# Kernel tuning notes

Measured on AMD Instinct MI355X. Metric: run time of the kernel, lower is better.

The kernel has to match this reference:

```python
import jax, jax.numpy as jnp
import numpy as np
import math

B, S, H, NH = 2, 2048, 1024, 16
HD = H // NH


def setup_inputs() -> dict:
    key = jax.random.key(0)
    k1, k2, k3 = jax.random.split(key, 3)
    hidden_states = jax.random.normal(k1, (B, S, H), dtype=jnp.float32)
    attention_mask = jnp.zeros((B, 1, 1, S), dtype=jnp.float32)
    w_qkv = jax.random.normal(k2, (3 * H, H), dtype=jnp.float32) * (1.0 / math.sqrt(H))
    w_out = jax.random.normal(k3, (H, H), dtype=jnp.float32) * (1.0 / math.sqrt(H))
    gate = jnp.ones((NH,), dtype=jnp.float32)
    return {"hidden_states": hidden_states, "attention_mask": attention_mask,
            "w_qkv": w_qkv, "w_out": w_out, "gate": gate}


def reference(hidden_states, attention_mask, w_qkv, w_out, gate):
    b, s, h = hidden_states.shape
    nh, hd = NH, HD
    # fused QKV projection (no bias)
    qkv = hidden_states @ w_qkv.T                      # [b, s, 3h]
    qkv = qkv.reshape(b, s, 3, nh, hd)
    q, k, v = jnp.moveaxis(qkv, 2, 0)                  # each [b, s, nh, hd]
    q = q.transpose(0, 2, 1, 3)                        # [b, nh, s, hd]
    k = k.transpose(0, 2, 1, 3)
    v = v.transpose(0, 2, 1, 3)
    scores = jnp.einsum('bhqd,bhkd->bhqk', q, k) / math.sqrt(hd)
    scores = scores + attention_mask                   # broadcast [b,1,1,s]
    probs = jax.nn.softmax(scores, axis=-1)            # dropout p=0 -> identity
    ctx = jnp.einsum('bhqk,bhkd->bhqd', probs, v)      # [b, nh, s, hd]
    ctx = ctx.transpose(0, 2, 1, 3)                    # [b, s, nh, hd]
    ctx = ctx * gate[None, None, :, None]              # per-head gating
    ctx = ctx.reshape(b, s, h)
    out = ctx @ w_out.T
    # all gates active (> 1e-4) -> active_gates/num_heads == 1, no rescale
    return out
```

## Files before the change

### kernel.cpp

```cpp
#include <hip/hip_runtime.h>
#include <stdint.h>


typedef __attribute__((ext_vector_type(8))) short short8;
typedef __attribute__((ext_vector_type(4))) float floatx4;
typedef __attribute__((ext_vector_type(4))) unsigned int uint4v;
typedef __attribute__((ext_vector_type(2))) unsigned int uint2v;

__device__ __forceinline__ unsigned short f2bf(float f) {
    unsigned int u = __float_as_uint(f);
    unsigned int r = u + 0x7fffu + ((u >> 16) & 1u);
    return (unsigned short)(r >> 16);
}
#if __has_builtin(__builtin_amdgcn_cvt_pk_bf16_f32)
__device__ __forceinline__ unsigned int pack_bf2(float lo, float hi) {
    auto v = __builtin_amdgcn_cvt_pk_bf16_f32(lo, hi);
    return __builtin_bit_cast(unsigned int, v);
}
#else
__device__ __forceinline__ unsigned int pack_bf2(float lo, float hi) {
    unsigned int a = __float_as_uint(lo) + 0x8000u;
    unsigned int b = __float_as_uint(hi) + 0x8000u;
    return __builtin_amdgcn_perm(b, a, 0x07060302u);
}
#endif

#if __has_builtin(__builtin_amdgcn_exp2f)
#define EXP2(x) __builtin_amdgcn_exp2f(x)
#else
#define EXP2(x) exp2f(x)
#endif

__device__ __forceinline__ void gl2lds16(const void* g, void* l) {
    __builtin_amdgcn_global_load_lds(
        (const __attribute__((address_space(1))) unsigned int*)g,
        (__attribute__((address_space(3))) unsigned int*)l, 16, 0, 0);
}

#define MFMA32(a, b, c) __builtin_amdgcn_mfma_f32_16x16x32_bf16((a), (b), (c), 0, 0, 0)

__global__ __launch_bounds__(256)
void cvt_all(const float* __restrict__ a, const float* __restrict__ b,
             const float* __restrict__ c, const float* __restrict__ mask,
             unsigned short* __restrict__ oa, unsigned short* __restrict__ ob,
             unsigned short* __restrict__ oc, float* __restrict__ m2b)
{
    int i = blockIdx.x * 256 + threadIdx.x;
    if (i >= 2097152) {
        int off = i - 2097152;
        float4 v = *(const float4*)(mask + (size_t)off * 4);
        const float L2E = 1.44269504f, C2 = -14.4269504f;
        float4 w;
        w.x = fmaf(v.x, L2E, C2); w.y = fmaf(v.y, L2E, C2);
        w.z = fmaf(v.z, L2E, C2); w.w = fmaf(v.w, L2E, C2);
        *(float4*)(m2b + (size_t)off * 4) = w;
        return;
    }
    const float* src; unsigned short* dst; int off;
    if (i < 1048576)      { src = a; dst = oa; off = i; }
    else if (i < 1835008) { src = b; dst = ob; off = i - 1048576; }
    else                  { src = c; dst = oc; off = i - 1835008; }
    float4 v = *(const float4*)(src + (size_t)off * 4);
    uint2v w;
    w[0] = pack_bf2(v.x, v.y);
    w[1] = pack_bf2(v.z, v.w);
    *(uint2v*)(dst + (size_t)off * 4) = w;
}

template<int MODE, int BN>
__global__ __launch_bounds__(256)
void gemm_nt(const unsigned short* __restrict__ A,
             const unsigned short* __restrict__ Bm,
             unsigned short* __restrict__ out0,
             unsigned short* __restrict__ out1,
             unsigned short* __restrict__ out2,
             float* __restrict__ outf,
             int N)
{
    constexpr int BUFB  = 8192 + BN * 64;
    constexpr int NSTEP = 32;
    constexpr int NA    = 2;
    constexpr int NB    = BN / 64;
    constexpr int BSL   = BN / 32;
    __shared__ unsigned char smem[3 * BUFB];
    const int K = 1024;
    const int tid  = threadIdx.x;
    const int wave = tid >> 6, lane = tid & 63;
    const int l15  = lane & 15, quad = lane >> 4;
    const int wm = wave >> 1, wn = wave & 1;

    int Lid = blockIdx.y * gridDim.x + blockIdx.x;
    int bm = (Lid & 7) * 4 + ((Lid >> 3) & 3);
    int bn = Lid >> 5;

    floatx4 acc[4][BSL];
#pragma unroll
    for (int i = 0; i < 4; i++)
#pragma unroll
        for (int j = 0; j < BSL; j++)
            acc[i][j] = floatx4{0.f, 0.f, 0.f, 0.f};

    int soffA[NA], soffB[NB];
#pragma unroll
    for (int l = 0; l < NA; l++) {
        int s = (wave * NA + l) * 64 + lane;
        int L = s >> 3, q = (s & 7) ^ (L & 7);
        soffA[l] = (L * 2 + (q >> 2)) * K + (q & 3) * 8;
    }
#pragma unroll
    for (int l = 0; l < NB; l++) {
        int s = (wave * NB + l) * 64 + lane;
        int L = s >> 3, q = (s & 7) ^ (L & 7);
        soffB[l] = (L * 2 + (q >> 2)) * K + (q & 3) * 8;
    }
    int aoff[4], boff[BSL];
#pragma unroll
    for (int i = 0; i < 4; i++) {
        int r = wm * 64 + i * 16 + l15, L = r >> 1;
        aoff[i] = L * 128 + (((((r & 1) << 2) | quad) ^ (L & 7)) * 16);
    }
#pragma unroll
    for (int j = 0; j < BSL; j++) {
        int r = wn * (BN / 2) + j * 16 + l15, L = r >> 1;
        boff[j] = 8192 + L * 128 + (((((r & 1) << 2) | quad) ^ (L & 7)) * 16);
    }

    const unsigned short* Abase = A  + (size_t)(bm * 128) * K;
    const unsigned short* Bbase = Bm + (size_t)(bn * BN) * K;

    auto STAGE = [&](int u, int bufb) {
        const int k0 = u * 32;
#pragma unroll
        for (int l = 0; l < NA; l++)
            gl2lds16(Abase + (size_t)soffA[l] + k0, &smem[bufb + (wave * NA + l) * 1024]);
#pragma unroll
        for (int l = 0; l < NB; l++)
            gl2lds16(Bbase + (size_t)soffB[l] + k0, &smem[bufb + 8192 + (wave * NB + l) * 1024]);
    };

    STAGE(0, 0);
    STAGE(1, BUFB);

    int b0 = 0, b2 = 2;
    for (int t = 0; t < NSTEP; t++) {
        asm volatile("" ::: "memory");
        __builtin_amdgcn_s_barrier();
        asm volatile("" ::: "memory");
        if (t + 2 < NSTEP) {
            STAGE(t + 2, b2 * BUFB);
            if (BN == 128) asm volatile("s_waitcnt vmcnt(8)" ::: "memory");
            else           asm volatile("s_waitcnt vmcnt(6)" ::: "memory");
        } else if (t + 2 == NSTEP) {
            if (BN == 128) asm volatile("s_waitcnt vmcnt(4)" ::: "memory");
            else           asm volatile("s_waitcnt vmcnt(3)" ::: "memory");
        } else {
            asm volatile("s_waitcnt vmcnt(0)" ::: "memory");
        }
        __builtin_amdgcn_s_barrier();
        asm volatile("" ::: "memory");

        const int cb = b0 * BUFB;
        short8 af[4], bfr[BSL];
#pragma unroll
        for (int i = 0; i < 4; i++)
            af[i] = *(const short8*)(&smem[cb + aoff[i]]);
#pragma unroll
        for (int j = 0; j < BSL; j++)
            bfr[j] = *(const short8*)(&smem[cb + boff[j]]);
#pragma unroll
        for (int i = 0; i < 4; i++)
#pragma unroll
            for (int j = 0; j < BSL; j++)
                acc[i][j] = MFMA32(af[i], bfr[j], acc[i][j]);

        b0 = (b0 == 2) ? 0 : b0 + 1;
        b2 = (b2 == 2) ? 0 : b2 + 1;
    }

#pragma unroll
    for (int i = 0; i < 4; i++) {
#pragma unroll
        for (int j = 0; j < BSL; j++) {
            int n = bn * BN + wn * (BN / 2) + j * 16 + l15;
#pragma unroll
            for (int r = 0; r < 4; r++) {
                int m = bm * 128 + wm * 64 + i * 16 + quad * 4 + r;
                float fv = acc[i][j][r];
                if (MODE == 1) {
                    outf[(size_t)m * N + n] = fv;
                } else {
                    int t = n >> 10;
                    int h = (n >> 6) & 15;
                    int d = n & 63;
                    int b = m >> 11, si = m & 2047;
                    if (t == 2) {
                        int sip = (si & ~31) | (((si >> 2) & 3) << 3)
                                | (((si >> 4) & 1) << 2) | (si & 3);
                        out2[(((size_t)(b * 16 + h)) * 64 + d) * 2048 + sip] = f2bf(fv);
                    } else {
                        if (t == 0) fv *= 0.18033688f;
                        size_t off = (((size_t)(b * 16 + h)) * 2048 + si) * 64 + d;
                        unsigned short* dst = (t == 0) ? out0 : out1;
                        dst[off] = f2bf(fv);
                    }
                }
            }
        }
    }
}

__global__ __launch_bounds__(256, 2)
void attn_kernel(const unsigned short* __restrict__ Qb,
                 const unsigned short* __restrict__ Kb,
                 const unsigned short* __restrict__ VbT,
                 const float* __restrict__ m2b,
                 const float* __restrict__ gateb,
                 unsigned short* __restrict__ ctx)
{
    __shared__ unsigned char smem[16384];
    const int S = 2048;
    const int tid  = threadIdx.x;
    const int wave = tid >> 6, lane = tid & 63;
    const int l15  = lane & 15, quad = lane >> 4;

    int Lid = blockIdx.y * gridDim.x + blockIdx.x;
    int bh = (Lid & 7) * 4 + ((Lid >> 3) & 3);
    int qc = Lid >> 5;
    const int b = bh >> 4, h = bh & 15;
    const int q0 = qc * 128 + wave * 32;

    const size_t headoff = (size_t)bh * S * 64;
    const unsigned short* Qh  = Qb  + headoff;
    const unsigned short* Kh  = Kb  + headoff;
    const unsigned short* VhT = VbT + headoff;
    const float* m2p = m2b + (size_t)b * S;

    int koff, voff;
    {
        int s = wave * 64 + lane;
        int key = s >> 3;
        koff = key * 64 + (((s & 7) ^ (key & 7)) * 8);
        int L = s >> 3, q = (s & 7) ^ (L & 7);
        voff = (L * 2 + (q >> 2)) * 2048 + (q & 3) * 8;
    }
    int qkoff[2];
#pragma unroll
    for (int s2 = 0; s2 < 2; s2++)
        qkoff[s2] = l15 * 128 + (((s2 * 4 + quad) ^ (l15 & 7)) * 16);
    const int pvoff = 4096 + (l15 >> 1) * 128
                    + (((((l15 & 1) << 2) | quad) ^ ((l15 >> 1) & 7)) * 16);

    short8 aq[2][2];
#pragma unroll
    for (int sub = 0; sub < 2; sub++)
#pragma unroll
        for (int s2 = 0; s2 < 2; s2++)
            aq[sub][s2] = *(const short8*)(Qh + (size_t)(q0 + sub * 16 + l15) * 64 + s2 * 32 + quad * 8);

    floatx4 o[2][4];
    floatx4 lq[2];
#pragma unroll
    for (int sub = 0; sub < 2; sub++) {
        lq[sub] = floatx4{0.f, 0.f, 0.f, 0.f};
#pragma unroll
        for (int dt = 0; dt < 4; dt++) o[sub][dt] = floatx4{0.f, 0.f, 0.f, 0.f};
    }

    const uint4v onesu = {0x3F803F80u, 0x3F803F80u, 0x3F803F80u, 0x3F803F80u};
    const short8 ONES = __builtin_bit_cast(short8, onesu);

    gl2lds16(Kh + koff, &smem[wave * 1024]);
    gl2lds16(VhT + voff, &smem[4096 + wave * 1024]);

    for (int i = 0; i < 64; i++) {
        const int cb = (i & 1) * 8192;
        const int nb = ((i + 1) & 1) * 8192;
        const int kb = i * 32;
        floatx4 mf[2];
#pragma unroll
        for (int t = 0; t < 2; t++)
            mf[t] = *(const floatx4*)(m2p + kb + t * 16 + quad * 4);
        asm volatile("" ::: "memory");
        __builtin_amdgcn_s_barrier();
        asm volatile("" ::: "memory");
        if (i + 1 < 64) {
            const int kbn = (i + 1) * 32;
            gl2lds16(Kh + (size_t)kbn * 64 + koff, &smem[nb + wave * 1024]);
            gl2lds16(VhT + kbn + voff, &smem[nb + 4096 + wave * 1024]);
            asm volatile("s_waitcnt vmcnt(2)" ::: "memory");
        } else {
            asm volatile("s_waitcnt vmcnt(0)" ::: "memory");
        }
        __builtin_amdgcn_s_barrier();
        asm volatile("" ::: "memory");

        short8 kf[2][2];
#pragma unroll
        for (int t = 0; t < 2; t++)
#pragma unroll
            for (int s2 = 0; s2 < 2; s2++)
                kf[t][s2] = *(const short8*)(&smem[cb + qkoff[s2] + t * 2048]);
        short8 vf[4];
#pragma unroll
        for (int dt = 0; dt < 4; dt++)
            vf[dt] = *(const short8*)(&smem[cb + pvoff + dt * 1024]);

#pragma unroll
        for (int sub = 0; sub < 2; sub++) {
            floatx4 st0 = MFMA32(kf[0][0], aq[sub][0], mf[0]);
            floatx4 st1 = MFMA32(kf[1][0], aq[sub][0], mf[1]);
            st0 = MFMA32(kf[0][1], aq[sub][1], st0);
            st1 = MFMA32(kf[1][1], aq[sub][1], st1);
            float e00 = EXP2(st0[0]), e01 = EXP2(st0[1]);
            float e02 = EXP2(st0[2]), e03 = EXP2(st0[3]);
            float e10 = EXP2(st1[0]), e11 = EXP2(st1[1]);
            float e12 = EXP2(st1[2]), e13 = EXP2(st1[3]);
            uint4v pu = {pack_bf2(e00, e01), pack_bf2(e02, e03),
                         pack_bf2(e10, e11), pack_bf2(e12, e13)};
            short8 pf = __builtin_bit_cast(short8, pu);
#pragma unroll
            for (int dt = 0; dt < 4; dt++)
                o[sub][dt] = MFMA32(vf[dt], pf, o[sub][dt]);
            lq[sub] = MFMA32(ONES, pf, lq[sub]);
        }
    }

    float g = gateb[h];
#pragma unroll
    for (int sub = 0; sub < 2; sub++) {
        float iv = g / lq[sub][0];
        size_t base = ((size_t)(b * 2048 + q0 + sub * 16 + l15)) * 1024 + h * 64 + quad * 4;
#pragma unroll
        for (int dt = 0; dt < 4; dt++) {
            uint2v w;
            w[0] = pack_bf2(o[sub][dt][0] * iv, o[sub][dt][1] * iv);
            w[1] = pack_bf2(o[sub][dt][2] * iv, o[sub][dt][3] * iv);
            *(uint2v*)(ctx + base + dt * 16) = w;
        }
    }
}

extern "C" void kernel_launch(void* const* d_in, const int* in_sizes, int n_in,
                              void* d_out, int out_size, void* d_ws, size_t ws_size,
                              hipStream_t stream)
{
    const float* hidden = (const float*)d_in[0];
    const float* mask   = (const float*)d_in[1];
    const float* w_qkv  = (const float*)d_in[2];
    const float* w_out  = (const float*)d_in[3];
    const float* gate   = (const float*)d_in[4];
    float* out = (float*)d_out;

    unsigned short* q_buf = (unsigned short*)d_ws;
    unsigned short* k_buf = q_buf + 4194304;
    unsigned short* v_buf = k_buf + 4194304;
    unsigned short* c_buf = v_buf + 4194304;
    unsigned short* h_bf  = c_buf + 4194304;
    unsigned short* wq_bf = h_bf  + 4194304;
    unsigned short* wo_bf = wq_bf + 3145728;
    float* m2_buf = (float*)(wo_bf + 1048576);

    cvt_all<<<8196, 256, 0, stream>>>(hidden, w_qkv, w_out, mask,
                                      h_bf, wq_bf, wo_bf, m2_buf);

    gemm_nt<0, 128><<<dim3(24, 32), 256, 0, stream>>>(h_bf, wq_bf, q_buf, k_buf, v_buf, nullptr, 3072);
    attn_kernel<<<dim3(16, 32), 256, 0, stream>>>(q_buf, k_buf, v_buf, m2_buf, gate, c_buf);
    gemm_nt<1, 64><<<dim3(16, 32), 256, 0, stream>>>(c_buf, wo_bf, nullptr, nullptr, nullptr, out, 1024);
}
```

Baseline: 188.3 us.

## Restructure attention kernel to 2-wave blocks with 64-key tiles and phased MFMA

Shrinks each attention workgroup to two waves covering 64 queries, doubles the grid, and processes 64 keys per iteration instead of 32, with a 32KB double-buffered LDS tile. The QK MFMAs, the exp/pack step and the PV MFMAs now run as separate phases, and s_setprio raises wave priority around the MFMA phases. The aim is to halve the barrier and loop overhead per key and improve MFMA issue overlap. The cost is more registers for the score, K and V fragments, larger LDS use per block, and a different V layout in LDS that relies on the transposed V buffer matching the new addressing.

```diff
diff --git a/kernel.cpp b/kernel.cpp
--- a/kernel.cpp
+++ b/kernel.cpp
@@ -209,7 +209,7 @@
     }
 }
 
-__global__ __launch_bounds__(256, 2)
+__global__ __launch_bounds__(128, 2)
 void attn_kernel(const unsigned short* __restrict__ Qb,
                  const unsigned short* __restrict__ Kb,
                  const unsigned short* __restrict__ VbT,
@@ -217,7 +217,7 @@
                  const float* __restrict__ gateb,
                  unsigned short* __restrict__ ctx)
 {
-    __shared__ unsigned char smem[16384];
+    __shared__ unsigned char smem[32768];
     const int S = 2048;
     const int tid  = threadIdx.x;
     const int wave = tid >> 6, lane = tid & 63;
@@ -227,7 +227,7 @@
     int bh = (Lid & 7) * 4 + ((Lid >> 3) & 3);
     int qc = Lid >> 5;
     const int b = bh >> 4, h = bh & 15;
-    const int q0 = qc * 128 + wave * 32;
+    const int q0 = qc * 64 + wave * 32;
 
     const size_t headoff = (size_t)bh * S * 64;
     const unsigned short* Qh  = Qb  + headoff;
@@ -235,20 +235,18 @@
     const unsigned short* VhT = VbT + headoff;
     const float* m2p = m2b + (size_t)b * S;
 
-    int koff, voff;
-    {
-        int s = wave * 64 + lane;
-        int key = s >> 3;
-        koff = key * 64 + (((s & 7) ^ (key & 7)) * 8);
-        int L = s >> 3, q = (s & 7) ^ (L & 7);
-        voff = (L * 2 + (q >> 2)) * 2048 + (q & 3) * 8;
+    int koff[4], voff[4];
+#pragma unroll
+    for (int l = 0; l < 4; l++) {
+        int s = (wave * 4 + l) * 64 + lane;
+        int L = s >> 3, c = (s & 7) ^ (L & 7);
+        koff[l] = L * 64 + c * 8;
+        voff[l] = L * 2048 + c * 8;
     }
     int qkoff[2];
 #pragma unroll
-    for (int s2 = 0; s2 < 2; s2++)
-        qkoff[s2] = l15 * 128 + (((s2 * 4 + quad) ^ (l15 & 7)) * 16);
-    const int pvoff = 4096 + (l15 >> 1) * 128
-                    + (((((l15 & 1) << 2) | quad) ^ ((l15 >> 1) & 7)) * 16);
+    for (int j = 0; j < 2; j++)
+        qkoff[j] = l15 * 128 + (((j * 4 + quad) ^ (l15 & 7)) * 16);
 
     short8 aq[2][2];
 #pragma unroll
@@ -269,60 +267,86 @@
     const uint4v onesu = {0x3F803F80u, 0x3F803F80u, 0x3F803F80u, 0x3F803F80u};
     const short8 ONES = __builtin_bit_cast(short8, onesu);
 
-    gl2lds16(Kh + koff, &smem[wave * 1024]);
-    gl2lds16(VhT + voff, &smem[4096 + wave * 1024]);
-
-    for (int i = 0; i < 64; i++) {
-        const int cb = (i & 1) * 8192;
-        const int nb = ((i + 1) & 1) * 8192;
-        const int kb = i * 32;
-        floatx4 mf[2];
-#pragma unroll
-        for (int t = 0; t < 2; t++)
+#pragma unroll
+    for (int l = 0; l < 4; l++) {
+        gl2lds16(Kh + koff[l], &smem[(wave * 4 + l) * 1024]);
+        gl2lds16(VhT + voff[l], &smem[8192 + (wave * 4 + l) * 1024]);
+    }
+
+    for (int i = 0; i < 32; i++) {
+        const int cb = (i & 1) * 16384;
+        const int nb = ((i + 1) & 1) * 16384;
+        const int kb = i * 64;
+        floatx4 mf[4];
+#pragma unroll
+        for (int t = 0; t < 4; t++)
             mf[t] = *(const floatx4*)(m2p + kb + t * 16 + quad * 4);
         asm volatile("" ::: "memory");
         __builtin_amdgcn_s_barrier();
         asm volatile("" ::: "memory");
-        if (i + 1 < 64) {
-            const int kbn = (i + 1) * 32;
-            gl2lds16(Kh + (size_t)kbn * 64 + koff, &smem[nb + wave * 1024]);
-            gl2lds16(VhT + kbn + voff, &smem[nb + 4096 + wave * 1024]);
-            asm volatile("s_waitcnt vmcnt(2)" ::: "memory");
+        if (i + 1 < 32) {
+            const int kbn = (i + 1) * 64;
+#pragma unroll
+            for (int l = 0; l < 4; l++) {
+                gl2lds16(Kh + (size_t)kbn * 64 + koff[l], &smem[nb + (wave * 4 + l) * 1024]);
+                gl2lds16(VhT + kbn + voff[l], &smem[nb + 8192 + (wave * 4 + l) * 1024]);
+            }
+            asm volatile("s_waitcnt vmcnt(8)" ::: "memory");
         } else {
             asm volatile("s_waitcnt vmcnt(0)" ::: "memory");
         }
         __builtin_amdgcn_s_barrier();
         asm volatile("" ::: "memory");
 
-        short8 kf[2][2];
-#pragma unroll
-        for (int t = 0; t < 2; t++)
+        short8 kf[4][2];
+#pragma unroll
+        for (int kt = 0; kt < 4; kt++)
 #pragma unroll
             for (int s2 = 0; s2 < 2; s2++)
-                kf[t][s2] = *(const short8*)(&smem[cb + qkoff[s2] + t * 2048]);
-        short8 vf[4];
+                kf[kt][s2] = *(const short8*)(&smem[cb + kt * 2048 + qkoff[s2]]);
+
+        floatx4 st[2][4];
+        __builtin_amdgcn_s_setprio(1);
+#pragma unroll
+        for (int sub = 0; sub < 2; sub++)
+#pragma unroll
+            for (int kt = 0; kt < 4; kt++) {
+                st[sub][kt] = MFMA32(kf[kt][0], aq[sub][0], mf[kt]);
+                st[sub][kt] = MFMA32(kf[kt][1], aq[sub][1], st[sub][kt]);
+            }
+        __builtin_amdgcn_s_setprio(0);
+
+        short8 vf[4][2];
 #pragma unroll
         for (int dt = 0; dt < 4; dt++)
-            vf[dt] = *(const short8*)(&smem[cb + pvoff + dt * 1024]);
-
-#pragma unroll
-        for (int sub = 0; sub < 2; sub++) {
-            floatx4 st0 = MFMA32(kf[0][0], aq[sub][0], mf[0]);
-            floatx4 st1 = MFMA32(kf[1][0], aq[sub][0], mf[1]);
-            st0 = MFMA32(kf[0][1], aq[sub][1], st0);
-            st1 = MFMA32(kf[1][1], aq[sub][1], st1);
-            float e00 = EXP2(st0[0]), e01 = EXP2(st0[1]);
-            float e02 = EXP2(st0[2]), e03 = EXP2(st0[3]);
-            float e10 = EXP2(st1[0]), e11 = EXP2(st1[1]);
-            float e12 = EXP2(st1[2]), e13 = EXP2(st1[3]);
-            uint4v pu = {pack_bf2(e00, e01), pack_bf2(e02, e03),
-                         pack_bf2(e10, e11), pack_bf2(e12, e13)};
-            short8 pf = __builtin_bit_cast(short8, pu);
-#pragma unroll
-            for (int dt = 0; dt < 4; dt++)
-                o[sub][dt] = MFMA32(vf[dt], pf, o[sub][dt]);
-            lq[sub] = MFMA32(ONES, pf, lq[sub]);
-        }
+#pragma unroll
+            for (int g = 0; g < 2; g++)
+                vf[dt][g] = *(const short8*)(&smem[cb + 8192 + dt * 2048 + qkoff[g]]);
+
+        short8 pf[2][2];
+#pragma unroll
+        for (int sub = 0; sub < 2; sub++)
+#pragma unroll
+            for (int g = 0; g < 2; g++) {
+                floatx4 a = st[sub][2 * g], c = st[sub][2 * g + 1];
+                uint4v pu = {pack_bf2(EXP2(a[0]), EXP2(a[1])),
+                             pack_bf2(EXP2(a[2]), EXP2(a[3])),
+                             pack_bf2(EXP2(c[0]), EXP2(c[1])),
+                             pack_bf2(EXP2(c[2]), EXP2(c[3]))};
+                pf[sub][g] = __builtin_bit_cast(short8, pu);
+            }
+
+        __builtin_amdgcn_s_setprio(1);
+#pragma unroll
+        for (int sub = 0; sub < 2; sub++)
+#pragma unroll
+            for (int g = 0; g < 2; g++) {
+#pragma unroll
+                for (int dt = 0; dt < 4; dt++)
+                    o[sub][dt] = MFMA32(vf[dt][g], pf[sub][g], o[sub][dt]);
+                lq[sub] = MFMA32(ONES, pf[sub][g], lq[sub]);
+            }
+        __builtin_amdgcn_s_setprio(0);
     }
 
     float g = gateb[h];
@@ -364,6 +388,6 @@
                                       h_bf, wq_bf, wo_bf, m2_buf);
 
     gemm_nt<0, 128><<<dim3(24, 32), 256, 0, stream>>>(h_bf, wq_bf, q_buf, k_buf, v_buf, nullptr, 3072);
-    attn_kernel<<<dim3(16, 32), 256, 0, stream>>>(q_buf, k_buf, v_buf, m2_buf, gate, c_buf);
+    attn_kernel<<<dim3(32, 32), 128, 0, stream>>>(q_buf, k_buf, v_buf, m2_buf, gate, c_buf);
     gemm_nt<1, 64><<<dim3(16, 32), 256, 0, stream>>>(c_buf, wo_bf, nullptr, nullptr, nullptr, out, 1024);
 }
```

New measurement: 194.2 us. 1.03x slower.
